# Kernel optimization log

Measured on AMD Instinct MI355X. Metric: run time of the kernel, lower is better.

## Reference

```python
import jax, jax.numpy as jnp
import numpy as np

QUERY_SIZE = 512
KEY_SIZE = 512
VALUE_SIZE = 512
HIDDEN = 128


def setup_inputs() -> dict:
    key = jax.random.key(0)
    ks = jax.random.split(key, 9)
    b, t_q, t_k = 8, 128, 512
    query = jax.random.normal(ks[0], (b, t_q, QUERY_SIZE), dtype=jnp.float32)
    keys = jax.random.normal(ks[1], (b, t_k, KEY_SIZE), dtype=jnp.float32)
    values = jax.random.normal(ks[2], (b, t_k, VALUE_SIZE), dtype=jnp.float32)
    # torch nn.Linear init ~ U(-1/sqrt(fan_in), 1/sqrt(fan_in)); scale-matched normals are fine
    sq = 1.0 / np.sqrt(QUERY_SIZE)
    sk = 1.0 / np.sqrt(KEY_SIZE)
    sh = 1.0 / np.sqrt(HIDDEN)
    Wq = jax.random.uniform(ks[3], (HIDDEN, QUERY_SIZE), jnp.float32, -sq, sq)
    bq = jax.random.uniform(ks[4], (HIDDEN,), jnp.float32, -sq, sq)
    Wk = jax.random.uniform(ks[5], (HIDDEN, KEY_SIZE), jnp.float32, -sk, sk)
    bk = jax.random.uniform(ks[6], (HIDDEN,), jnp.float32, -sk, sk)
    Wo = jax.random.uniform(ks[7], (1, HIDDEN), jnp.float32, -sh, sh)
    bo = jax.random.uniform(ks[8], (1,), jnp.float32, -sh, sh)
    return {"query": query, "keys": keys, "values": values,
            "Wq": Wq, "bq": bq, "Wk": Wk, "bk": bk, "Wo": Wo, "bo": bo}


def reference(query, keys, values, Wq, bq, Wk, bk, Wo, bo):
    # Bahdanau additive attention: att_ij = Wo @ tanh(Wq q_i + Wk k_j + bq + bk) + bo
    # Project once per position (mathematically identical to the expanded per-pair Linear).
    q_proj = jnp.einsum('bqn,hn->bqh', query, Wq) + bq          # b x t_q x h
    k_proj = jnp.einsum('bkn,hn->bkh', keys, Wk) + bk           # b x t_k x h
    hid = jnp.tanh(q_proj[:, :, None, :] + k_proj[:, None, :, :])  # b x t_q x t_k x h
    scores = jnp.einsum('bqkh,h->bqk', hid, Wo[0]) + bo[0]       # b x t_q x t_k
    attn = jax.nn.softmax(scores, axis=2)
    context = jnp.einsum('bqk,bkv->bqv', attn, values)           # b x t_q x n_v
    return context, attn
```

## Files before the change

### kernel.cpp

```cpp
#include <hip/hip_runtime.h>


#define B_    8
#define TQ_   128
#define TK_   512
#define NIN_  512
#define H_    128
#define NV_   512
#define NQR   (B_*TQ_)
#define NROWS (NQR + B_*TK_)

#define C2_   2.8853900817779268f
#define L2E_  1.4426950408889634f

__device__ __forceinline__ float fexp2(float x){ return __builtin_amdgcn_exp2f(x); }
__device__ __forceinline__ float frcp (float x){ return __builtin_amdgcn_rcpf(x); }

__global__ __launch_bounds__(128, 4) void proj_kernel(
        const float* __restrict__ query, const float* __restrict__ keys,
        const float* __restrict__ Wq, const float* __restrict__ bq,
        const float* __restrict__ Wk, const float* __restrict__ bk,
        float* __restrict__ qp, float* __restrict__ kp) {
    __shared__ float at[32][20];
    __shared__ float wt[32][68];
    const int tid = threadIdx.x;
    const int r0  = (blockIdx.x >> 1) * 16;
    const int h0  = (blockIdx.x & 1) * 64;
    const float* in; const float* W; const float* bias; float* outp;
    if (r0 < NQR) {
        in = query + (size_t)r0 * NIN_; W = Wq; bias = bq;
        outp = qp + (size_t)r0 * H_;
    } else {
        const int rk = r0 - NQR;
        in = keys + (size_t)rk * NIN_;  W = Wk; bias = bk;
        outp = kp + (size_t)rk * H_;
    }

    const int r2  = (tid >> 4) * 2;
    const int h4l = (tid & 15) * 4;
    const int sr  = tid >> 3;
    const int skq = (tid & 7) * 4;

    const float* pA  = in + (size_t)sr * NIN_ + skq;
    const float* pW0 = W + (size_t)(h0 + sr     ) * NIN_ + skq;
    const float* pW1 = W + (size_t)(h0 + sr + 16) * NIN_ + skq;
    const float* pW2 = W + (size_t)(h0 + sr + 32) * NIN_ + skq;
    const float* pW3 = W + (size_t)(h0 + sr + 48) * NIN_ + skq;

    float4 af = *(const float4*)pA;
    float4 w0 = *(const float4*)pW0, w1 = *(const float4*)pW1;
    float4 w2 = *(const float4*)pW2, w3 = *(const float4*)pW3;

    float acc[2][4] = {{0.f,0.f,0.f,0.f},{0.f,0.f,0.f,0.f}};

    for (int c = 0; c < 16; ++c) {
        __syncthreads();
        at[skq+0][sr] = af.x; at[skq+1][sr] = af.y;
        at[skq+2][sr] = af.z; at[skq+3][sr] = af.w;
        wt[skq+0][sr   ] = w0.x; wt[skq+1][sr   ] = w0.y;
        wt[skq+2][sr   ] = w0.z; wt[skq+3][sr   ] = w0.w;
        wt[skq+0][sr+16] = w1.x; wt[skq+1][sr+16] = w1.y;
        wt[skq+2][sr+16] = w1.z; wt[skq+3][sr+16] = w1.w;
        wt[skq+0][sr+32] = w2.x; wt[skq+1][sr+32] = w2.y;
        wt[skq+2][sr+32] = w2.z; wt[skq+3][sr+32] = w2.w;
        wt[skq+0][sr+48] = w3.x; wt[skq+1][sr+48] = w3.y;
        wt[skq+2][sr+48] = w3.z; wt[skq+3][sr+48] = w3.w;
        __syncthreads();
        if (c + 1 < 16) {
            pA += 32; pW0 += 32; pW1 += 32; pW2 += 32; pW3 += 32;
            af = *(const float4*)pA;
            w0 = *(const float4*)pW0; w1 = *(const float4*)pW1;
            w2 = *(const float4*)pW2; w3 = *(const float4*)pW3;
        }
#pragma unroll 8
        for (int kk = 0; kk < 32; ++kk) {
            const float2 a = *(const float2*)&at[kk][r2];
            const float4 w = *(const float4*)&wt[kk][h4l];
            acc[0][0] = fmaf(a.x, w.x, acc[0][0]);
            acc[0][1] = fmaf(a.x, w.y, acc[0][1]);
            acc[0][2] = fmaf(a.x, w.z, acc[0][2]);
            acc[0][3] = fmaf(a.x, w.w, acc[0][3]);
            acc[1][0] = fmaf(a.y, w.x, acc[1][0]);
            acc[1][1] = fmaf(a.y, w.y, acc[1][1]);
            acc[1][2] = fmaf(a.y, w.z, acc[1][2]);
            acc[1][3] = fmaf(a.y, w.w, acc[1][3]);
        }
    }

    const float4 b4 = *(const float4*)&bias[h0 + h4l];
#pragma unroll
    for (int i = 0; i < 2; ++i) {
        float4 o = {(acc[i][0] + b4.x) * C2_, (acc[i][1] + b4.y) * C2_,
                    (acc[i][2] + b4.z) * C2_, (acc[i][3] + b4.w) * C2_};
        *(float4*)&outp[(size_t)(r2 + i) * H_ + h0 + h4l] = o;
    }
}

__global__ __launch_bounds__(256, 4) void scores_kernel(
        const float* __restrict__ qp, const float* __restrict__ kp,
        const float* __restrict__ Wo, const float* __restrict__ bo,
        float* __restrict__ out_attn) {
    __shared__ float qs2[2][H_];
    __shared__ float w2[H_];
    __shared__ float sc[2][TK_];

    const int tid = threadIdx.x;
    const int b   = blockIdx.y;
    const int q0  = blockIdx.x * 2;
    const int lane = tid & 63;

    qs2[tid >> 7][tid & 127] =
        qp[(size_t)(b * TQ_ + q0 + (tid >> 7)) * H_ + (tid & 127)];
    if (tid < H_) w2[tid] = Wo[tid] * -2.0f;
    __syncthreads();

    float sw = w2[lane] + w2[lane + 64];
#pragma unroll
    for (int m = 1; m < 64; m <<= 1) sw += __shfl_xor(sw, m);
    const float sbase = bo[0] - 0.5f * sw;

#pragma unroll
    for (int half = 0; half < 2; ++half) {
        const int k = tid + half * 256;
        const float4* kp4 = (const float4*)&kp[(size_t)(b * TK_ + k) * H_];
        float s0 = 0.f, s1 = 0.f;
#pragma unroll 4
        for (int hb = 0; hb < 32; ++hb) {
            const float4 kv  = kp4[hb];
            const float4 wv  = *(const float4*)&w2[hb * 4];
            const float4 q0v = *(const float4*)&qs2[0][hb * 4];
            const float4 q1v = *(const float4*)&qs2[1][hb * 4];
            s0 = fmaf(wv.x, frcp(fexp2(q0v.x + kv.x) + 1.f), s0);
            s0 = fmaf(wv.y, frcp(fexp2(q0v.y + kv.y) + 1.f), s0);
            s0 = fmaf(wv.z, frcp(fexp2(q0v.z + kv.z) + 1.f), s0);
            s0 = fmaf(wv.w, frcp(fexp2(q0v.w + kv.w) + 1.f), s0);
            s1 = fmaf(wv.x, frcp(fexp2(q1v.x + kv.x) + 1.f), s1);
            s1 = fmaf(wv.y, frcp(fexp2(q1v.y + kv.y) + 1.f), s1);
            s1 = fmaf(wv.z, frcp(fexp2(q1v.z + kv.z) + 1.f), s1);
            s1 = fmaf(wv.w, frcp(fexp2(q1v.w + kv.w) + 1.f), s1);
        }
        sc[0][k] = s0 + sbase;
        sc[1][k] = s1 + sbase;
    }
    __syncthreads();

    const int w = tid >> 6;
    if (w < 2) {
        float4 sA = *(const float4*)&sc[w][lane * 8];
        float4 sB = *(const float4*)&sc[w][lane * 8 + 4];
        float m = fmaxf(fmaxf(fmaxf(sA.x, sA.y), fmaxf(sA.z, sA.w)),
                        fmaxf(fmaxf(sB.x, sB.y), fmaxf(sB.z, sB.w)));
#pragma unroll
        for (int mk = 1; mk < 64; mk <<= 1) m = fmaxf(m, __shfl_xor(m, mk));
        float4 eA, eB;
        eA.x = fexp2((sA.x - m) * L2E_); eA.y = fexp2((sA.y - m) * L2E_);
        eA.z = fexp2((sA.z - m) * L2E_); eA.w = fexp2((sA.w - m) * L2E_);
        eB.x = fexp2((sB.x - m) * L2E_); eB.y = fexp2((sB.y - m) * L2E_);
        eB.z = fexp2((sB.z - m) * L2E_); eB.w = fexp2((sB.w - m) * L2E_);
        float s = eA.x + eA.y + eA.z + eA.w + eB.x + eB.y + eB.z + eB.w;
#pragma unroll
        for (int mk = 1; mk < 64; mk <<= 1) s += __shfl_xor(s, mk);
        const float inv = frcp(s);
        eA.x *= inv; eA.y *= inv; eA.z *= inv; eA.w *= inv;
        eB.x *= inv; eB.y *= inv; eB.z *= inv; eB.w *= inv;
        float4* op = (float4*)&out_attn[(size_t)(b * TQ_ + q0 + w) * TK_ + lane * 8];
        op[0] = eA; op[1] = eB;
    }
}

__global__ __launch_bounds__(128, 4) void context_kernel(
        const float* __restrict__ attn, const float* __restrict__ values,
        float* __restrict__ outc) {
    __shared__ float at[32][12];
    __shared__ float vt[32][68];

    const int tid = threadIdx.x;
    const int b   = blockIdx.y;
    const int q0  = (blockIdx.x >> 3) * 8;
    const int v0  = (blockIdx.x & 7) * 64;

    const int v2 = (tid & 31) * 2;
    const int q2 = (tid >> 5) * 2;
    const int ar  = tid >> 3;
    const int akq = (tid & 7) * 4;
    const int vr  = tid >> 4;
    const int vq  = (tid & 15) * 4;

    const float* pAt = attn + (size_t)(b * TQ_ + q0 + ar) * TK_ + akq;
    const float* pV0 = values + (size_t)(b * TK_ + vr     ) * NV_ + v0 + vq;
    const float* pV1 = values + (size_t)(b * TK_ + vr +  8) * NV_ + v0 + vq;
    const float* pV2 = values + (size_t)(b * TK_ + vr + 16) * NV_ + v0 + vq;
    const float* pV3 = values + (size_t)(b * TK_ + vr + 24) * NV_ + v0 + vq;

    float4 af = {0.f,0.f,0.f,0.f};
    if (tid < 64) af = *(const float4*)pAt;
    float4 vf0 = *(const float4*)pV0;
    float4 vf1 = *(const float4*)pV1;
    float4 vf2 = *(const float4*)pV2;
    float4 vf3 = *(const float4*)pV3;

    float acc[2][2] = {{0.f,0.f},{0.f,0.f}};

    for (int c = 0; c < 16; ++c) {
        __syncthreads();
        if (tid < 64) {
            at[akq+0][ar] = af.x; at[akq+1][ar] = af.y;
            at[akq+2][ar] = af.z; at[akq+3][ar] = af.w;
        }
        *(float4*)&vt[vr     ][vq] = vf0;
        *(float4*)&vt[vr +  8][vq] = vf1;
        *(float4*)&vt[vr + 16][vq] = vf2;
        *(float4*)&vt[vr + 24][vq] = vf3;
        __syncthreads();
        if (c + 1 < 16) {
            pAt += 32; pV0 += 32 * NV_; pV1 += 32 * NV_;
            pV2 += 32 * NV_; pV3 += 32 * NV_;
            if (tid < 64) af = *(const float4*)pAt;
            vf0 = *(const float4*)pV0; vf1 = *(const float4*)pV1;
            vf2 = *(const float4*)pV2; vf3 = *(const float4*)pV3;
        }
#pragma unroll 8
        for (int kk = 0; kk < 32; ++kk) {
            const float2 a = *(const float2*)&at[kk][q2];
            const float2 v = *(const float2*)&vt[kk][v2];
            acc[0][0] = fmaf(a.x, v.x, acc[0][0]);
            acc[0][1] = fmaf(a.x, v.y, acc[0][1]);
            acc[1][0] = fmaf(a.y, v.x, acc[1][0]);
            acc[1][1] = fmaf(a.y, v.y, acc[1][1]);
        }
    }
    float2 o0 = {acc[0][0], acc[0][1]};
    float2 o1 = {acc[1][0], acc[1][1]};
    *(float2*)&outc[(size_t)(b * TQ_ + q0 + q2 + 0) * NV_ + v0 + v2] = o0;
    *(float2*)&outc[(size_t)(b * TQ_ + q0 + q2 + 1) * NV_ + v0 + v2] = o1;
}

extern "C" void kernel_launch(void* const* d_in, const int* in_sizes, int n_in,
                              void* d_out, int out_size, void* d_ws, size_t ws_size,
                              hipStream_t stream) {
    const float* query  = (const float*)d_in[0];
    const float* keys   = (const float*)d_in[1];
    const float* values = (const float*)d_in[2];
    const float* Wq     = (const float*)d_in[3];
    const float* bq     = (const float*)d_in[4];
    const float* Wk     = (const float*)d_in[5];
    const float* bk     = (const float*)d_in[6];
    const float* Wo     = (const float*)d_in[7];
    const float* bo     = (const float*)d_in[8];

    float* out_ctx  = (float*)d_out;
    float* out_attn = out_ctx + B_ * TQ_ * NV_;
    float* qp = (float*)d_ws;
    float* kp = qp + (size_t)NQR * H_;

    proj_kernel<<<dim3(NROWS / 16 * 2), 128, 0, stream>>>(
        query, keys, Wq, bq, Wk, bk, qp, kp);
    scores_kernel<<<dim3(TQ_ / 2, B_), 256, 0, stream>>>(qp, kp, Wo, bo, out_attn);
    context_kernel<<<dim3(128, B_), 128, 0, stream>>>(out_attn, values, out_ctx);
}
```

Measured before the change: 72.14 us.

## Split-K both projection and context GEMMs with separate reduction kernels

The projection GEMM now has each block cover all 128 hidden outputs for 16 rows, and its 512-wide reduction is split across 4 grid slices that write partial sums. A new kernel adds the partials, applies bias and scaling. The context GEMM is likewise split-K across 4 slices with a larger 2x4 per-thread tile, followed by a reduction kernel. The goal is more blocks and less serial K-loop per block, at the cost of extra workspace traffic and two more kernel launches.

```diff
diff --git a/kernel.cpp b/kernel.cpp
--- a/kernel.cpp
+++ b/kernel.cpp
@@ -9,6 +9,7 @@
 #define NV_   512
 #define NQR   (B_*TQ_)
 #define NROWS (NQR + B_*TK_)
+#define CTXN  (B_*TQ_*NV_)
 
 #define C2_   2.8853900817779268f
 #define L2E_  1.4426950408889634f
@@ -16,66 +17,61 @@
 __device__ __forceinline__ float fexp2(float x){ return __builtin_amdgcn_exp2f(x); }
 __device__ __forceinline__ float frcp (float x){ return __builtin_amdgcn_rcpf(x); }
 
-__global__ __launch_bounds__(128, 4) void proj_kernel(
+__global__ __launch_bounds__(256, 5) void proj_kernel(
         const float* __restrict__ query, const float* __restrict__ keys,
-        const float* __restrict__ Wq, const float* __restrict__ bq,
-        const float* __restrict__ Wk, const float* __restrict__ bk,
-        float* __restrict__ qp, float* __restrict__ kp) {
-    __shared__ float at[32][20];
-    __shared__ float wt[32][68];
-    const int tid = threadIdx.x;
-    const int r0  = (blockIdx.x >> 1) * 16;
-    const int h0  = (blockIdx.x & 1) * 64;
-    const float* in; const float* W; const float* bias; float* outp;
-    if (r0 < NQR) {
-        in = query + (size_t)r0 * NIN_; W = Wq; bias = bq;
-        outp = qp + (size_t)r0 * H_;
-    } else {
-        const int rk = r0 - NQR;
-        in = keys + (size_t)rk * NIN_;  W = Wk; bias = bk;
-        outp = kp + (size_t)rk * H_;
-    }
-
-    const int r2  = (tid >> 4) * 2;
-    const int h4l = (tid & 15) * 4;
-    const int sr  = tid >> 3;
-    const int skq = (tid & 7) * 4;
-
-    const float* pA  = in + (size_t)sr * NIN_ + skq;
-    const float* pW0 = W + (size_t)(h0 + sr     ) * NIN_ + skq;
-    const float* pW1 = W + (size_t)(h0 + sr + 16) * NIN_ + skq;
-    const float* pW2 = W + (size_t)(h0 + sr + 32) * NIN_ + skq;
-    const float* pW3 = W + (size_t)(h0 + sr + 48) * NIN_ + skq;
-
-    float4 af = *(const float4*)pA;
+        const float* __restrict__ Wq, const float* __restrict__ Wk,
+        float* __restrict__ psum, int kper) {
+    __shared__ float at[32][18];
+    __shared__ float wt[32][132];
+    const int tid = threadIdx.x;
+    const int r0  = blockIdx.x * 16;
+    const float* in; const float* W;
+    if (r0 < NQR) { in = query + (size_t)r0 * NIN_;         W = Wq; }
+    else          { in = keys  + (size_t)(r0 - NQR) * NIN_; W = Wk; }
+
+    const int r2 = (tid >> 5) * 2;
+    const int h4 = (tid & 31) * 4;
+    const int ar  = tid >> 4;
+    const int ak2 = (tid & 15) * 2;
+    const int wr  = tid >> 3;
+    const int wkq = (tid & 7) * 4;
+    const int kb0 = blockIdx.y * kper;
+    const int nc  = kper >> 5;
+
+    const float* pA  = in + (size_t)ar * NIN_ + kb0 + ak2;
+    const float* pW0 = W + (size_t)(wr     ) * NIN_ + kb0 + wkq;
+    const float* pW1 = W + (size_t)(wr + 32) * NIN_ + kb0 + wkq;
+    const float* pW2 = W + (size_t)(wr + 64) * NIN_ + kb0 + wkq;
+    const float* pW3 = W + (size_t)(wr + 96) * NIN_ + kb0 + wkq;
+
+    float2 af = *(const float2*)pA;
     float4 w0 = *(const float4*)pW0, w1 = *(const float4*)pW1;
     float4 w2 = *(const float4*)pW2, w3 = *(const float4*)pW3;
 
     float acc[2][4] = {{0.f,0.f,0.f,0.f},{0.f,0.f,0.f,0.f}};
 
-    for (int c = 0; c < 16; ++c) {
-        __syncthreads();
-        at[skq+0][sr] = af.x; at[skq+1][sr] = af.y;
-        at[skq+2][sr] = af.z; at[skq+3][sr] = af.w;
-        wt[skq+0][sr   ] = w0.x; wt[skq+1][sr   ] = w0.y;
-        wt[skq+2][sr   ] = w0.z; wt[skq+3][sr   ] = w0.w;
-        wt[skq+0][sr+16] = w1.x; wt[skq+1][sr+16] = w1.y;
-        wt[skq+2][sr+16] = w1.z; wt[skq+3][sr+16] = w1.w;
-        wt[skq+0][sr+32] = w2.x; wt[skq+1][sr+32] = w2.y;
-        wt[skq+2][sr+32] = w2.z; wt[skq+3][sr+32] = w2.w;
-        wt[skq+0][sr+48] = w3.x; wt[skq+1][sr+48] = w3.y;
-        wt[skq+2][sr+48] = w3.z; wt[skq+3][sr+48] = w3.w;
-        __syncthreads();
-        if (c + 1 < 16) {
+    for (int c = 0; c < nc; ++c) {
+        __syncthreads();
+        at[ak2+0][ar] = af.x; at[ak2+1][ar] = af.y;
+        wt[wkq+0][wr   ] = w0.x; wt[wkq+1][wr   ] = w0.y;
+        wt[wkq+2][wr   ] = w0.z; wt[wkq+3][wr   ] = w0.w;
+        wt[wkq+0][wr+32] = w1.x; wt[wkq+1][wr+32] = w1.y;
+        wt[wkq+2][wr+32] = w1.z; wt[wkq+3][wr+32] = w1.w;
+        wt[wkq+0][wr+64] = w2.x; wt[wkq+1][wr+64] = w2.y;
+        wt[wkq+2][wr+64] = w2.z; wt[wkq+3][wr+64] = w2.w;
+        wt[wkq+0][wr+96] = w3.x; wt[wkq+1][wr+96] = w3.y;
+        wt[wkq+2][wr+96] = w3.z; wt[wkq+3][wr+96] = w3.w;
+        __syncthreads();
+        if (c + 1 < nc) {
             pA += 32; pW0 += 32; pW1 += 32; pW2 += 32; pW3 += 32;
-            af = *(const float4*)pA;
+            af = *(const float2*)pA;
             w0 = *(const float4*)pW0; w1 = *(const float4*)pW1;
             w2 = *(const float4*)pW2; w3 = *(const float4*)pW3;
         }
 #pragma unroll 8
         for (int kk = 0; kk < 32; ++kk) {
             const float2 a = *(const float2*)&at[kk][r2];
-            const float4 w = *(const float4*)&wt[kk][h4l];
+            const float4 w = *(const float4*)&wt[kk][h4];
             acc[0][0] = fmaf(a.x, w.x, acc[0][0]);
             acc[0][1] = fmaf(a.x, w.y, acc[0][1]);
             acc[0][2] = fmaf(a.x, w.z, acc[0][2]);
@@ -87,13 +83,29 @@
         }
     }
 
-    const float4 b4 = *(const float4*)&bias[h0 + h4l];
+    float* op = psum + ((size_t)blockIdx.y * NROWS + r0) * H_;
 #pragma unroll
     for (int i = 0; i < 2; ++i) {
-        float4 o = {(acc[i][0] + b4.x) * C2_, (acc[i][1] + b4.y) * C2_,
-                    (acc[i][2] + b4.z) * C2_, (acc[i][3] + b4.w) * C2_};
-        *(float4*)&outp[(size_t)(r2 + i) * H_ + h0 + h4l] = o;
-    }
+        float4 o = {acc[i][0], acc[i][1], acc[i][2], acc[i][3]};
+        *(float4*)&op[(size_t)(r2 + i) * H_ + h4] = o;
+    }
+}
+
+__global__ __launch_bounds__(256, 4) void reduceP_kernel(
+        const float* __restrict__ psum, const float* __restrict__ bq,
+        const float* __restrict__ bk, float* __restrict__ pout) {
+    const int tid = threadIdx.x;
+    const int r0  = blockIdx.x * 8;
+    const float* bias = (r0 < NQR) ? bq : bk;
+    const int row = tid >> 5, hq = (tid & 31) * 4;
+    float4 s = *(const float4*)&bias[hq];
+#pragma unroll
+    for (int sp = 0; sp < 4; ++sp) {
+        float4 v = *(const float4*)&psum[((size_t)sp * NROWS + r0 + row) * H_ + hq];
+        s.x += v.x; s.y += v.y; s.z += v.z; s.w += v.w;
+    }
+    float4 o = {s.x * C2_, s.y * C2_, s.z * C2_, s.w * C2_};
+    *(float4*)&pout[(size_t)(r0 + row) * H_ + hq] = o;
 }
 
 __global__ __launch_bounds__(256, 4) void scores_kernel(
@@ -170,69 +182,86 @@
 
 __global__ __launch_bounds__(128, 4) void context_kernel(
         const float* __restrict__ attn, const float* __restrict__ values,
-        float* __restrict__ outc) {
-    __shared__ float at[32][12];
+        float* __restrict__ psumC) {
+    __shared__ float at[32][18];
     __shared__ float vt[32][68];
 
     const int tid = threadIdx.x;
-    const int b   = blockIdx.y;
-    const int q0  = (blockIdx.x >> 3) * 8;
-    const int v0  = (blockIdx.x & 7) * 64;
-
-    const int v2 = (tid & 31) * 2;
-    const int q2 = (tid >> 5) * 2;
+    const int r0  = blockIdx.x * 16;
+    const int b   = r0 >> 7;
+    const int v0  = blockIdx.y * 64;
+    const int kb0 = blockIdx.z * 128;
+
+    const int q2 = (tid >> 4) * 2;
+    const int v4 = (tid & 15) * 4;
     const int ar  = tid >> 3;
     const int akq = (tid & 7) * 4;
     const int vr  = tid >> 4;
     const int vq  = (tid & 15) * 4;
 
-    const float* pAt = attn + (size_t)(b * TQ_ + q0 + ar) * TK_ + akq;
-    const float* pV0 = values + (size_t)(b * TK_ + vr     ) * NV_ + v0 + vq;
-    const float* pV1 = values + (size_t)(b * TK_ + vr +  8) * NV_ + v0 + vq;
-    const float* pV2 = values + (size_t)(b * TK_ + vr + 16) * NV_ + v0 + vq;
-    const float* pV3 = values + (size_t)(b * TK_ + vr + 24) * NV_ + v0 + vq;
-
-    float4 af = {0.f,0.f,0.f,0.f};
-    if (tid < 64) af = *(const float4*)pAt;
+    const float* pAt = attn + (size_t)(r0 + ar) * TK_ + kb0 + akq;
+    const float* pV0 = values + (size_t)(b * TK_ + kb0 + vr     ) * NV_ + v0 + vq;
+    const float* pV1 = values + (size_t)(b * TK_ + kb0 + vr +  8) * NV_ + v0 + vq;
+    const float* pV2 = values + (size_t)(b * TK_ + kb0 + vr + 16) * NV_ + v0 + vq;
+    const float* pV3 = values + (size_t)(b * TK_ + kb0 + vr + 24) * NV_ + v0 + vq;
+
+    float4 af  = *(const float4*)pAt;
     float4 vf0 = *(const float4*)pV0;
     float4 vf1 = *(const float4*)pV1;
     float4 vf2 = *(const float4*)pV2;
     float4 vf3 = *(const float4*)pV3;
 
-    float acc[2][2] = {{0.f,0.f},{0.f,0.f}};
-
-    for (int c = 0; c < 16; ++c) {
-        __syncthreads();
-        if (tid < 64) {
-            at[akq+0][ar] = af.x; at[akq+1][ar] = af.y;
-            at[akq+2][ar] = af.z; at[akq+3][ar] = af.w;
-        }
+    float acc[2][4] = {{0.f,0.f,0.f,0.f},{0.f,0.f,0.f,0.f}};
+
+    for (int c = 0; c < 4; ++c) {
+        __syncthreads();
+        at[akq+0][ar] = af.x; at[akq+1][ar] = af.y;
+        at[akq+2][ar] = af.z; at[akq+3][ar] = af.w;
         *(float4*)&vt[vr     ][vq] = vf0;
         *(float4*)&vt[vr +  8][vq] = vf1;
         *(float4*)&vt[vr + 16][vq] = vf2;
         *(float4*)&vt[vr + 24][vq] = vf3;
         __syncthreads();
-        if (c + 1 < 16) {
+        if (c + 1 < 4) {
             pAt += 32; pV0 += 32 * NV_; pV1 += 32 * NV_;
             pV2 += 32 * NV_; pV3 += 32 * NV_;
-            if (tid < 64) af = *(const float4*)pAt;
+            af  = *(const float4*)pAt;
             vf0 = *(const float4*)pV0; vf1 = *(const float4*)pV1;
             vf2 = *(const float4*)pV2; vf3 = *(const float4*)pV3;
         }
 #pragma unroll 8
         for (int kk = 0; kk < 32; ++kk) {
             const float2 a = *(const float2*)&at[kk][q2];
-            const float2 v = *(const float2*)&vt[kk][v2];
+            const float4 v = *(const float4*)&vt[kk][v4];
             acc[0][0] = fmaf(a.x, v.x, acc[0][0]);
             acc[0][1] = fmaf(a.x, v.y, acc[0][1]);
+            acc[0][2] = fmaf(a.x, v.z, acc[0][2]);
+            acc[0][3] = fmaf(a.x, v.w, acc[0][3]);
             acc[1][0] = fmaf(a.y, v.x, acc[1][0]);
             acc[1][1] = fmaf(a.y, v.y, acc[1][1]);
-        }
-    }
-    float2 o0 = {acc[0][0], acc[0][1]};
-    float2 o1 = {acc[1][0], acc[1][1]};
-    *(float2*)&outc[(size_t)(b * TQ_ + q0 + q2 + 0) * NV_ + v0 + v2] = o0;
-    *(float2*)&outc[(size_t)(b * TQ_ + q0 + q2 + 1) * NV_ + v0 + v2] = o1;
+            acc[1][2] = fmaf(a.y, v.z, acc[1][2]);
+            acc[1][3] = fmaf(a.y, v.w, acc[1][3]);
+        }
+    }
+
+    float* op = psumC + (size_t)blockIdx.z * CTXN + (size_t)r0 * NV_ + v0;
+#pragma unroll
+    for (int i = 0; i < 2; ++i) {
+        float4 o = {acc[i][0], acc[i][1], acc[i][2], acc[i][3]};
+        *(float4*)&op[(size_t)(q2 + i) * NV_ + v4] = o;
+    }
+}
+
+__global__ __launch_bounds__(256, 4) void reduceC_kernel(
+        const float* __restrict__ psumC, float* __restrict__ outc) {
+    const size_t i = ((size_t)blockIdx.x * 256 + threadIdx.x) * 4;
+    float4 s = *(const float4*)&psumC[i];
+#pragma unroll
+    for (int z = 1; z < 4; ++z) {
+        float4 v = *(const float4*)&psumC[(size_t)z * CTXN + i];
+        s.x += v.x; s.y += v.y; s.z += v.z; s.w += v.w;
+    }
+    *(float4*)&outc[i] = s;
 }
 
 extern "C" void kernel_launch(void* const* d_in, const int* in_sizes, int n_in,
@@ -250,11 +279,17 @@
 
     float* out_ctx  = (float*)d_out;
     float* out_attn = out_ctx + B_ * TQ_ * NV_;
-    float* qp = (float*)d_ws;
-    float* kp = qp + (size_t)NQR * H_;
-
-    proj_kernel<<<dim3(NROWS / 16 * 2), 128, 0, stream>>>(
-        query, keys, Wq, bq, Wk, bk, qp, kp);
+    float* pout  = (float*)d_ws;
+    float* qp    = pout;
+    float* kp    = pout + (size_t)NQR * H_;
+    float* psumP = pout + (size_t)NROWS * H_;
+    float* psumC = psumP + (size_t)4 * NROWS * H_;
+
+    proj_kernel<<<dim3(NROWS / 16, 4), 256, 0, stream>>>(
+        query, keys, Wq, Wk, psumP, NIN_ / 4);
+    reduceP_kernel<<<NROWS / 8, 256, 0, stream>>>(psumP, bq, bk, pout);
     scores_kernel<<<dim3(TQ_ / 2, B_), 256, 0, stream>>>(qp, kp, Wo, bo, out_attn);
-    context_kernel<<<dim3(128, B_), 128, 0, stream>>>(out_attn, values, out_ctx);
-}
+    context_kernel<<<dim3(NQR / 16, NV_ / 64, 4), 128, 0, stream>>>(
+        out_attn, values, psumC);
+    reduceC_kernel<<<CTXN / 1024, 256, 0, stream>>>(psumC, out_ctx);
+}
```

New measurement: 66.10 us. -8.4%, faster.

## Fuse all stages into one persistent kernel with grid-wide atomic barriers

Applied to the files above, without the earlier changes.

Merges the projection, scores/softmax and context kernels into a single 512-block persistent kernel. Stages are separated by software grid barriers built on atomic counters, which are reset with a memset before each launch. The projection now uses split-K into four partial buffers plus a reduction pass, and the context stage moves to a direct global-load loop over values. This removes launch gaps and raises parallelism in the projection. In exchange it pays for barrier spin costs and extra partial-sum traffic, and it can deadlock unless all 512 blocks are co-resident.

```diff
diff --git a/kernel.cpp b/kernel.cpp
--- a/kernel.cpp
+++ b/kernel.cpp
@@ -9,6 +9,7 @@
 #define NV_   512
 #define NQR   (B_*TQ_)
 #define NROWS (NQR + B_*TK_)
+#define GRID_ 512
 
 #define C2_   2.8853900817779268f
 #define L2E_  1.4426950408889634f
@@ -16,223 +17,231 @@
 __device__ __forceinline__ float fexp2(float x){ return __builtin_amdgcn_exp2f(x); }
 __device__ __forceinline__ float frcp (float x){ return __builtin_amdgcn_rcpf(x); }
 
-__global__ __launch_bounds__(128, 4) void proj_kernel(
+union Smem {
+    struct { float at[32][36]; float wt[32][132]; } p;
+    struct { float qs2[2][H_]; float w2[H_]; float sc[2][TK_]; } s;
+    struct { float a[8][TK_]; } c;
+};
+
+__device__ __forceinline__ void gbar(unsigned* bar, int i) {
+    __syncthreads();
+    if (threadIdx.x == 0) {
+        __threadfence();
+        __hip_atomic_fetch_add(&bar[i], 1u, __ATOMIC_ACQ_REL,
+                               __HIP_MEMORY_SCOPE_AGENT);
+        while (__hip_atomic_load(&bar[i], __ATOMIC_ACQUIRE,
+                                 __HIP_MEMORY_SCOPE_AGENT) < GRID_)
+            __builtin_amdgcn_s_sleep(2);
+        __threadfence();
+    }
+    __syncthreads();
+}
+
+__global__ __launch_bounds__(256, 2) void fused_kernel(
         const float* __restrict__ query, const float* __restrict__ keys,
+        const float* __restrict__ values,
         const float* __restrict__ Wq, const float* __restrict__ bq,
         const float* __restrict__ Wk, const float* __restrict__ bk,
-        float* __restrict__ qp, float* __restrict__ kp) {
-    __shared__ float at[32][20];
-    __shared__ float wt[32][68];
+        const float* __restrict__ Wo, const float* __restrict__ bo,
+        float* __restrict__ psum, float* __restrict__ pout,
+        float* __restrict__ out_ctx, float* __restrict__ out_attn,
+        unsigned* __restrict__ bar) {
+    __shared__ Smem sm;
     const int tid = threadIdx.x;
-    const int r0  = (blockIdx.x >> 1) * 16;
-    const int h0  = (blockIdx.x & 1) * 64;
-    const float* in; const float* W; const float* bias; float* outp;
-    if (r0 < NQR) {
-        in = query + (size_t)r0 * NIN_; W = Wq; bias = bq;
-        outp = qp + (size_t)r0 * H_;
-    } else {
-        const int rk = r0 - NQR;
-        in = keys + (size_t)rk * NIN_;  W = Wk; bias = bk;
-        outp = kp + (size_t)rk * H_;
-    }
-
-    const int r2  = (tid >> 4) * 2;
-    const int h4l = (tid & 15) * 4;
-    const int sr  = tid >> 3;
-    const int skq = (tid & 7) * 4;
-
-    const float* pA  = in + (size_t)sr * NIN_ + skq;
-    const float* pW0 = W + (size_t)(h0 + sr     ) * NIN_ + skq;
-    const float* pW1 = W + (size_t)(h0 + sr + 16) * NIN_ + skq;
-    const float* pW2 = W + (size_t)(h0 + sr + 32) * NIN_ + skq;
-    const float* pW3 = W + (size_t)(h0 + sr + 48) * NIN_ + skq;
-
-    float4 af = *(const float4*)pA;
-    float4 w0 = *(const float4*)pW0, w1 = *(const float4*)pW1;
-    float4 w2 = *(const float4*)pW2, w3 = *(const float4*)pW3;
-
-    float acc[2][4] = {{0.f,0.f,0.f,0.f},{0.f,0.f,0.f,0.f}};
-
-    for (int c = 0; c < 16; ++c) {
+    const int bid = blockIdx.x;
+
+    {
+        const int r4  = (tid >> 5) * 4;
+        const int h4  = (tid & 31) * 4;
+        const int sr  = tid >> 3;
+        const int skq = (tid & 7) * 4;
+        for (int t = bid; t < 640; t += GRID_) {
+            const int s    = t / 160;
+            const int tile = t - s * 160;
+            const int r0   = tile * 32;
+            const int kb0  = s * 128;
+            const float* in; const float* W;
+            if (r0 < NQR) { in = query + (size_t)r0 * NIN_;         W = Wq; }
+            else          { in = keys  + (size_t)(r0 - NQR) * NIN_; W = Wk; }
+
+            const float* pA  = in + (size_t)sr * NIN_ + kb0 + skq;
+            const float* pW0 = W + (size_t)(sr     ) * NIN_ + kb0 + skq;
+            const float* pW1 = W + (size_t)(sr + 32) * NIN_ + kb0 + skq;
+            const float* pW2 = W + (size_t)(sr + 64) * NIN_ + kb0 + skq;
+            const float* pW3 = W + (size_t)(sr + 96) * NIN_ + kb0 + skq;
+
+            float4 af = *(const float4*)pA;
+            float4 w0 = *(const float4*)pW0, w1 = *(const float4*)pW1;
+            float4 w2 = *(const float4*)pW2, w3 = *(const float4*)pW3;
+
+            float acc[4][4];
+#pragma unroll
+            for (int i = 0; i < 4; ++i)
+#pragma unroll
+                for (int j = 0; j < 4; ++j) acc[i][j] = 0.0f;
+
+            for (int c = 0; c < 4; ++c) {
+                __syncthreads();
+                sm.p.at[skq+0][sr] = af.x; sm.p.at[skq+1][sr] = af.y;
+                sm.p.at[skq+2][sr] = af.z; sm.p.at[skq+3][sr] = af.w;
+                sm.p.wt[skq+0][sr   ] = w0.x; sm.p.wt[skq+1][sr   ] = w0.y;
+                sm.p.wt[skq+2][sr   ] = w0.z; sm.p.wt[skq+3][sr   ] = w0.w;
+                sm.p.wt[skq+0][sr+32] = w1.x; sm.p.wt[skq+1][sr+32] = w1.y;
+                sm.p.wt[skq+2][sr+32] = w1.z; sm.p.wt[skq+3][sr+32] = w1.w;
+                sm.p.wt[skq+0][sr+64] = w2.x; sm.p.wt[skq+1][sr+64] = w2.y;
+                sm.p.wt[skq+2][sr+64] = w2.z; sm.p.wt[skq+3][sr+64] = w2.w;
+                sm.p.wt[skq+0][sr+96] = w3.x; sm.p.wt[skq+1][sr+96] = w3.y;
+                sm.p.wt[skq+2][sr+96] = w3.z; sm.p.wt[skq+3][sr+96] = w3.w;
+                __syncthreads();
+                if (c + 1 < 4) {
+                    pA += 32; pW0 += 32; pW1 += 32; pW2 += 32; pW3 += 32;
+                    af = *(const float4*)pA;
+                    w0 = *(const float4*)pW0; w1 = *(const float4*)pW1;
+                    w2 = *(const float4*)pW2; w3 = *(const float4*)pW3;
+                }
+#pragma unroll 8
+                for (int kk = 0; kk < 32; ++kk) {
+                    const float4 a = *(const float4*)&sm.p.at[kk][r4];
+                    const float4 w = *(const float4*)&sm.p.wt[kk][h4];
+                    const float av[4] = {a.x, a.y, a.z, a.w};
+                    const float wv[4] = {w.x, w.y, w.z, w.w};
+#pragma unroll
+                    for (int i = 0; i < 4; ++i)
+#pragma unroll
+                        for (int j = 0; j < 4; ++j)
+                            acc[i][j] = fmaf(av[i], wv[j], acc[i][j]);
+                }
+            }
+            float* op = psum + ((size_t)s * NROWS + r0) * H_;
+#pragma unroll
+            for (int i = 0; i < 4; ++i) {
+                float4 o = {acc[i][0], acc[i][1], acc[i][2], acc[i][3]};
+                *(float4*)&op[(size_t)(r4 + i) * H_ + h4] = o;
+            }
+        }
+    }
+    gbar(bar, 0);
+
+    {
+        for (int t = bid; t < 320; t += GRID_) {
+            const int r0 = t * 16;
+            const float* bias = (r0 < NQR) ? bq : bk;
+#pragma unroll
+            for (int p = 0; p < 2; ++p) {
+                const int j = tid + p * 256;
+                const int row = j >> 5, hq = (j & 31) * 4;
+                float4 sv = *(const float4*)&bias[hq];
+#pragma unroll
+                for (int sp = 0; sp < 4; ++sp) {
+                    const float4 v = *(const float4*)
+                        &psum[((size_t)sp * NROWS + r0 + row) * H_ + hq];
+                    sv.x += v.x; sv.y += v.y; sv.z += v.z; sv.w += v.w;
+                }
+                float4 o = {sv.x * C2_, sv.y * C2_, sv.z * C2_, sv.w * C2_};
+                *(float4*)&pout[(size_t)(r0 + row) * H_ + hq] = o;
+            }
+        }
+    }
+    gbar(bar, 1);
+
+    {
+        const int b    = bid >> 6;
+        const int q0   = (bid & 63) * 2;
+        const int lane = tid & 63;
+        const float* qp = pout;
+        const float* kp = pout + (size_t)NQR * H_;
+
+        sm.s.qs2[tid >> 7][tid & 127] =
+            qp[(size_t)(b * TQ_ + q0 + (tid >> 7)) * H_ + (tid & 127)];
+        if (tid < H_) sm.s.w2[tid] = Wo[tid] * -2.0f;
         __syncthreads();
-        at[skq+0][sr] = af.x; at[skq+1][sr] = af.y;
-        at[skq+2][sr] = af.z; at[skq+3][sr] = af.w;
-        wt[skq+0][sr   ] = w0.x; wt[skq+1][sr   ] = w0.y;
-        wt[skq+2][sr   ] = w0.z; wt[skq+3][sr   ] = w0.w;
-        wt[skq+0][sr+16] = w1.x; wt[skq+1][sr+16] = w1.y;
-        wt[skq+2][sr+16] = w1.z; wt[skq+3][sr+16] = w1.w;
-        wt[skq+0][sr+32] = w2.x; wt[skq+1][sr+32] = w2.y;
-        wt[skq+2][sr+32] = w2.z; wt[skq+3][sr+32] = w2.w;
-        wt[skq+0][sr+48] = w3.x; wt[skq+1][sr+48] = w3.y;
-        wt[skq+2][sr+48] = w3.z; wt[skq+3][sr+48] = w3.w;
+
+        float sw = sm.s.w2[lane] + sm.s.w2[lane + 64];
+#pragma unroll
+        for (int m = 1; m < 64; m <<= 1) sw += __shfl_xor(sw, m);
+        const float sbase = bo[0] - 0.5f * sw;
+
+#pragma unroll
+        for (int half = 0; half < 2; ++half) {
+            const int k = tid + half * 256;
+            const float4* kp4 = (const float4*)&kp[(size_t)(b * TK_ + k) * H_];
+            float s0 = 0.f, s1 = 0.f;
+#pragma unroll 4
+            for (int hb = 0; hb < 32; ++hb) {
+                const float4 kv  = kp4[hb];
+                const float4 wv  = *(const float4*)&sm.s.w2[hb * 4];
+                const float4 q0v = *(const float4*)&sm.s.qs2[0][hb * 4];
+                const float4 q1v = *(const float4*)&sm.s.qs2[1][hb * 4];
+                s0 = fmaf(wv.x, frcp(fexp2(q0v.x + kv.x) + 1.f), s0);
+                s0 = fmaf(wv.y, frcp(fexp2(q0v.y + kv.y) + 1.f), s0);
+                s0 = fmaf(wv.z, frcp(fexp2(q0v.z + kv.z) + 1.f), s0);
+                s0 = fmaf(wv.w, frcp(fexp2(q0v.w + kv.w) + 1.f), s0);
+                s1 = fmaf(wv.x, frcp(fexp2(q1v.x + kv.x) + 1.f), s1);
+                s1 = fmaf(wv.y, frcp(fexp2(q1v.y + kv.y) + 1.f), s1);
+                s1 = fmaf(wv.z, frcp(fexp2(q1v.z + kv.z) + 1.f), s1);
+                s1 = fmaf(wv.w, frcp(fexp2(q1v.w + kv.w) + 1.f), s1);
+            }
+            sm.s.sc[0][k] = s0 + sbase;
+            sm.s.sc[1][k] = s1 + sbase;
+        }
         __syncthreads();
-        if (c + 1 < 16) {
-            pA += 32; pW0 += 32; pW1 += 32; pW2 += 32; pW3 += 32;
-            af = *(const float4*)pA;
-            w0 = *(const float4*)pW0; w1 = *(const float4*)pW1;
-            w2 = *(const float4*)pW2; w3 = *(const float4*)pW3;
-        }
+
+        const int w = tid >> 6;
+        if (w < 2) {
+            float4 sA = *(const float4*)&sm.s.sc[w][lane * 8];
+            float4 sB = *(const float4*)&sm.s.sc[w][lane * 8 + 4];
+            float m = fmaxf(fmaxf(fmaxf(sA.x, sA.y), fmaxf(sA.z, sA.w)),
+                            fmaxf(fmaxf(sB.x, sB.y), fmaxf(sB.z, sB.w)));
+#pragma unroll
+            for (int mk = 1; mk < 64; mk <<= 1) m = fmaxf(m, __shfl_xor(m, mk));
+            float4 eA, eB;
+            eA.x = fexp2((sA.x - m) * L2E_); eA.y = fexp2((sA.y - m) * L2E_);
+            eA.z = fexp2((sA.z - m) * L2E_); eA.w = fexp2((sA.w - m) * L2E_);
+            eB.x = fexp2((sB.x - m) * L2E_); eB.y = fexp2((sB.y - m) * L2E_);
+            eB.z = fexp2((sB.z - m) * L2E_); eB.w = fexp2((sB.w - m) * L2E_);
+            float s = eA.x + eA.y + eA.z + eA.w + eB.x + eB.y + eB.z + eB.w;
+#pragma unroll
+            for (int mk = 1; mk < 64; mk <<= 1) s += __shfl_xor(s, mk);
+            const float inv = frcp(s);
+            eA.x *= inv; eA.y *= inv; eA.z *= inv; eA.w *= inv;
+            eB.x *= inv; eB.y *= inv; eB.z *= inv; eB.w *= inv;
+            float4* op = (float4*)
+                &out_attn[(size_t)(b * TQ_ + q0 + w) * TK_ + lane * 8];
+            op[0] = eA; op[1] = eB;
+        }
+    }
+    gbar(bar, 2);
+
+    {
+        const int v0 = (bid & 3) * 128;
+        const int qt = bid >> 2;
+        const int b  = qt >> 4;
+        const int q0 = (qt & 15) * 8;
+
+#pragma unroll
+        for (int p = 0; p < 4; ++p) {
+            const int idx = tid + p * 256;
+            const int row = idx >> 7, kq = (idx & 127) * 4;
+            *(float4*)&sm.c.a[row][kq] =
+                *(const float4*)&out_attn[(size_t)(b * TQ_ + q0 + row) * TK_ + kq];
+        }
+        __syncthreads();
+
+        const int q  = tid >> 5;
+        const int v4 = v0 + (tid & 31) * 4;
+        const float* vp = values + (size_t)b * TK_ * NV_ + v4;
+        float4 acc = {0.f, 0.f, 0.f, 0.f};
 #pragma unroll 8
-        for (int kk = 0; kk < 32; ++kk) {
-            const float2 a = *(const float2*)&at[kk][r2];
-            const float4 w = *(const float4*)&wt[kk][h4l];
-            acc[0][0] = fmaf(a.x, w.x, acc[0][0]);
-            acc[0][1] = fmaf(a.x, w.y, acc[0][1]);
-            acc[0][2] = fmaf(a.x, w.z, acc[0][2]);
-            acc[0][3] = fmaf(a.x, w.w, acc[0][3]);
-            acc[1][0] = fmaf(a.y, w.x, acc[1][0]);
-            acc[1][1] = fmaf(a.y, w.y, acc[1][1]);
-            acc[1][2] = fmaf(a.y, w.z, acc[1][2]);
-            acc[1][3] = fmaf(a.y, w.w, acc[1][3]);
-        }
-    }
-
-    const float4 b4 = *(const float4*)&bias[h0 + h4l];
-#pragma unroll
-    for (int i = 0; i < 2; ++i) {
-        float4 o = {(acc[i][0] + b4.x) * C2_, (acc[i][1] + b4.y) * C2_,
-                    (acc[i][2] + b4.z) * C2_, (acc[i][3] + b4.w) * C2_};
-        *(float4*)&outp[(size_t)(r2 + i) * H_ + h0 + h4l] = o;
-    }
-}
-
-__global__ __launch_bounds__(256, 4) void scores_kernel(
-        const float* __restrict__ qp, const float* __restrict__ kp,
-        const float* __restrict__ Wo, const float* __restrict__ bo,
-        float* __restrict__ out_attn) {
-    __shared__ float qs2[2][H_];
-    __shared__ float w2[H_];
-    __shared__ float sc[2][TK_];
-
-    const int tid = threadIdx.x;
-    const int b   = blockIdx.y;
-    const int q0  = blockIdx.x * 2;
-    const int lane = tid & 63;
-
-    qs2[tid >> 7][tid & 127] =
-        qp[(size_t)(b * TQ_ + q0 + (tid >> 7)) * H_ + (tid & 127)];
-    if (tid < H_) w2[tid] = Wo[tid] * -2.0f;
-    __syncthreads();
-
-    float sw = w2[lane] + w2[lane + 64];
-#pragma unroll
-    for (int m = 1; m < 64; m <<= 1) sw += __shfl_xor(sw, m);
-    const float sbase = bo[0] - 0.5f * sw;
-
-#pragma unroll
-    for (int half = 0; half < 2; ++half) {
-        const int k = tid + half * 256;
-        const float4* kp4 = (const float4*)&kp[(size_t)(b * TK_ + k) * H_];
-        float s0 = 0.f, s1 = 0.f;
-#pragma unroll 4
-        for (int hb = 0; hb < 32; ++hb) {
-            const float4 kv  = kp4[hb];
-            const float4 wv  = *(const float4*)&w2[hb * 4];
-            const float4 q0v = *(const float4*)&qs2[0][hb * 4];
-            const float4 q1v = *(const float4*)&qs2[1][hb * 4];
-            s0 = fmaf(wv.x, frcp(fexp2(q0v.x + kv.x) + 1.f), s0);
-            s0 = fmaf(wv.y, frcp(fexp2(q0v.y + kv.y) + 1.f), s0);
-            s0 = fmaf(wv.z, frcp(fexp2(q0v.z + kv.z) + 1.f), s0);
-            s0 = fmaf(wv.w, frcp(fexp2(q0v.w + kv.w) + 1.f), s0);
-            s1 = fmaf(wv.x, frcp(fexp2(q1v.x + kv.x) + 1.f), s1);
-            s1 = fmaf(wv.y, frcp(fexp2(q1v.y + kv.y) + 1.f), s1);
-            s1 = fmaf(wv.z, frcp(fexp2(q1v.z + kv.z) + 1.f), s1);
-            s1 = fmaf(wv.w, frcp(fexp2(q1v.w + kv.w) + 1.f), s1);
-        }
-        sc[0][k] = s0 + sbase;
-        sc[1][k] = s1 + sbase;
-    }
-    __syncthreads();
-
-    const int w = tid >> 6;
-    if (w < 2) {
-        float4 sA = *(const float4*)&sc[w][lane * 8];
-        float4 sB = *(const float4*)&sc[w][lane * 8 + 4];
-        float m = fmaxf(fmaxf(fmaxf(sA.x, sA.y), fmaxf(sA.z, sA.w)),
-                        fmaxf(fmaxf(sB.x, sB.y), fmaxf(sB.z, sB.w)));
-#pragma unroll
-        for (int mk = 1; mk < 64; mk <<= 1) m = fmaxf(m, __shfl_xor(m, mk));
-        float4 eA, eB;
-        eA.x = fexp2((sA.x - m) * L2E_); eA.y = fexp2((sA.y - m) * L2E_);
-        eA.z = fexp2((sA.z - m) * L2E_); eA.w = fexp2((sA.w - m) * L2E_);
-        eB.x = fexp2((sB.x - m) * L2E_); eB.y = fexp2((sB.y - m) * L2E_);
-        eB.z = fexp2((sB.z - m) * L2E_); eB.w = fexp2((sB.w - m) * L2E_);
-        float s = eA.x + eA.y + eA.z + eA.w + eB.x + eB.y + eB.z + eB.w;
-#pragma unroll
-        for (int mk = 1; mk < 64; mk <<= 1) s += __shfl_xor(s, mk);
-        const float inv = frcp(s);
-        eA.x *= inv; eA.y *= inv; eA.z *= inv; eA.w *= inv;
-        eB.x *= inv; eB.y *= inv; eB.z *= inv; eB.w *= inv;
-        float4* op = (float4*)&out_attn[(size_t)(b * TQ_ + q0 + w) * TK_ + lane * 8];
-        op[0] = eA; op[1] = eB;
-    }
-}
-
-__global__ __launch_bounds__(128, 4) void context_kernel(
-        const float* __restrict__ attn, const float* __restrict__ values,
-        float* __restrict__ outc) {
-    __shared__ float at[32][12];
-    __shared__ float vt[32][68];
-
-    const int tid = threadIdx.x;
-    const int b   = blockIdx.y;
-    const int q0  = (blockIdx.x >> 3) * 8;
-    const int v0  = (blockIdx.x & 7) * 64;
-
-    const int v2 = (tid & 31) * 2;
-    const int q2 = (tid >> 5) * 2;
-    const int ar  = tid >> 3;
-    const int akq = (tid & 7) * 4;
-    const int vr  = tid >> 4;
-    const int vq  = (tid & 15) * 4;
-
-    const float* pAt = attn + (size_t)(b * TQ_ + q0 + ar) * TK_ + akq;
-    const float* pV0 = values + (size_t)(b * TK_ + vr     ) * NV_ + v0 + vq;
-    const float* pV1 = values + (size_t)(b * TK_ + vr +  8) * NV_ + v0 + vq;
-    const float* pV2 = values + (size_t)(b * TK_ + vr + 16) * NV_ + v0 + vq;
-    const float* pV3 = values + (size_t)(b * TK_ + vr + 24) * NV_ + v0 + vq;
-
-    float4 af = {0.f,0.f,0.f,0.f};
-    if (tid < 64) af = *(const float4*)pAt;
-    float4 vf0 = *(const float4*)pV0;
-    float4 vf1 = *(const float4*)pV1;
-    float4 vf2 = *(const float4*)pV2;
-    float4 vf3 = *(const float4*)pV3;
-
-    float acc[2][2] = {{0.f,0.f},{0.f,0.f}};
-
-    for (int c = 0; c < 16; ++c) {
-        __syncthreads();
-        if (tid < 64) {
-            at[akq+0][ar] = af.x; at[akq+1][ar] = af.y;
-            at[akq+2][ar] = af.z; at[akq+3][ar] = af.w;
-        }
-        *(float4*)&vt[vr     ][vq] = vf0;
-        *(float4*)&vt[vr +  8][vq] = vf1;
-        *(float4*)&vt[vr + 16][vq] = vf2;
-        *(float4*)&vt[vr + 24][vq] = vf3;
-        __syncthreads();
-        if (c + 1 < 16) {
-            pAt += 32; pV0 += 32 * NV_; pV1 += 32 * NV_;
-            pV2 += 32 * NV_; pV3 += 32 * NV_;
-            if (tid < 64) af = *(const float4*)pAt;
-            vf0 = *(const float4*)pV0; vf1 = *(const float4*)pV1;
-            vf2 = *(const float4*)pV2; vf3 = *(const float4*)pV3;
-        }
-#pragma unroll 8
-        for (int kk = 0; kk < 32; ++kk) {
-            const float2 a = *(const float2*)&at[kk][q2];
-            const float2 v = *(const float2*)&vt[kk][v2];
-            acc[0][0] = fmaf(a.x, v.x, acc[0][0]);
-            acc[0][1] = fmaf(a.x, v.y, acc[0][1]);
-            acc[1][0] = fmaf(a.y, v.x, acc[1][0]);
-            acc[1][1] = fmaf(a.y, v.y, acc[1][1]);
-        }
-    }
-    float2 o0 = {acc[0][0], acc[0][1]};
-    float2 o1 = {acc[1][0], acc[1][1]};
-    *(float2*)&outc[(size_t)(b * TQ_ + q0 + q2 + 0) * NV_ + v0 + v2] = o0;
-    *(float2*)&outc[(size_t)(b * TQ_ + q0 + q2 + 1) * NV_ + v0 + v2] = o1;
+        for (int k = 0; k < TK_; ++k) {
+            const float4 vv = *(const float4*)&vp[(size_t)k * NV_];
+            const float a = sm.c.a[q][k];
+            acc.x = fmaf(a, vv.x, acc.x);
+            acc.y = fmaf(a, vv.y, acc.y);
+            acc.z = fmaf(a, vv.z, acc.z);
+            acc.w = fmaf(a, vv.w, acc.w);
+        }
+        *(float4*)&out_ctx[(size_t)(b * TQ_ + q0 + q) * NV_ + v4] = acc;
+    }
 }
 
 extern "C" void kernel_launch(void* const* d_in, const int* in_sizes, int n_in,
@@ -250,11 +259,13 @@
 
     float* out_ctx  = (float*)d_out;
     float* out_attn = out_ctx + B_ * TQ_ * NV_;
-    float* qp = (float*)d_ws;
-    float* kp = qp + (size_t)NQR * H_;
-
-    proj_kernel<<<dim3(NROWS / 16 * 2), 128, 0, stream>>>(
-        query, keys, Wq, bq, Wk, bk, qp, kp);
-    scores_kernel<<<dim3(TQ_ / 2, B_), 256, 0, stream>>>(qp, kp, Wo, bo, out_attn);
-    context_kernel<<<dim3(128, B_), 128, 0, stream>>>(out_attn, values, out_ctx);
+    unsigned* bar = (unsigned*)d_ws;
+    float* base = (float*)d_ws + 64;
+    float* psum = base;
+    float* pout = psum + (size_t)4 * NROWS * H_;
+
+    hipMemsetAsync(d_ws, 0, 64, stream);
+    fused_kernel<<<GRID_, 256, 0, stream>>>(
+        query, keys, values, Wq, bq, Wk, bk, Wo, bo,
+        psum, pout, out_ctx, out_attn, bar);
 }
```

Result: slower. 268.0 us (+271.5%).
